# Kernel optimization log

Measured on AMD Instinct MI355X. Metric: run time of the kernel, lower is better.

Reference implementation:

```python
import jax, jax.numpy as jnp
import numpy as np

ALPHA = 0.9
BETA = 1.0  # theta=None, layer=None -> PyG GCN2Conv beta = 1.0
N_CONV = 2


def _gcn_norm(edge_index, edge_weight, num_nodes):
    # gcn_norm with add_self_loops=False: symmetric D^-1/2 A D^-1/2
    row, col = edge_index[0], edge_index[1]
    deg = jax.ops.segment_sum(edge_weight, col, num_segments=num_nodes)
    dinv = jnp.where(deg > 0, jax.lax.rsqrt(jnp.where(deg > 0, deg, 1.0)), 0.0)
    return dinv[row] * edge_weight * dinv[col]


def _gcn2_conv(h, x0, edge_index, norm_w, w1, num_nodes):
    row, col = edge_index[0], edge_index[1]
    msg = h[row] * norm_w[:, None]                     # gather + scale  [E, F]
    agg = jax.ops.segment_sum(msg, col, num_segments=num_nodes)  # scatter-add [N, F]
    out = (1.0 - ALPHA) * agg + ALPHA * x0             # initial residual
    return (1.0 - BETA) * out + BETA * (out @ w1)      # shared_weights=True path


def setup_inputs() -> dict:
    key = jax.random.key(0)
    ks = jax.random.split(key, 8)
    N, E, H, F = 100000, 1600000, 64, 64
    x = jax.random.normal(ks[0], (N, H), dtype=jnp.float32)
    edge_index = jax.random.randint(ks[1], (2, E), 0, N, dtype=jnp.int64)
    edge_weight = jax.random.uniform(ks[2], (E,), dtype=jnp.float32)
    edge_attr = jax.random.normal(ks[3], (E, 5), dtype=jnp.float32)
    lin0_w = jax.random.normal(ks[4], (F, H), dtype=jnp.float32) / np.sqrt(H)
    lin0_b = jnp.zeros((F,), dtype=jnp.float32)
    # per-conv GCN2Conv weight1 [n_conv, F, F]
    w1 = jax.random.normal(ks[5], (N_CONV, F, F), dtype=jnp.float32) / np.sqrt(F)
    return {"x": x, "edge_index": edge_index, "edge_weight": edge_weight,
            "edge_attr": edge_attr, "lin0_w": lin0_w, "lin0_b": lin0_b, "w1": w1}


def reference(x, edge_index, edge_weight, edge_attr, lin0_w, lin0_b, w1):
    del edge_attr  # unused by the module
    num_nodes = x.shape[0]
    h0 = jax.nn.relu(x @ lin0_w.T + lin0_b)
    norm_w = _gcn_norm(edge_index, edge_weight, num_nodes)
    out = h0
    for i in range(N_CONV):
        out = out + jax.nn.relu(_gcn2_conv(out, h0, edge_index, norm_w, w1[i], num_nodes))
    return out
```

## Files before the change

kernel.cpp:

```cpp
#include <hip/hip_runtime.h>
#include <hip/hip_fp16.h>

#define NN 100000
#define NE 1600000
#define H0_NB 1563
#define HBLK 256
#define EPB 6250
#define NBKT 196
#define CAP 9216

static __device__ __forceinline__ float bitsf(unsigned u) {
    union { unsigned u; float f; } t; t.u = u; return t.f;
}

static __device__ __forceinline__ unsigned short f2bf(float f) {
    union { float f; unsigned u; } t; t.f = f;
    unsigned r = t.u + 0x7fffu + ((t.u >> 16) & 1u);
    return (unsigned short)(r >> 16);
}

static __device__ __forceinline__ void ld_bf4(const unsigned short* p, float* f) {
    uint2 u = *reinterpret_cast<const uint2*>(p);
    f[0] = bitsf(u.x << 16);
    f[1] = bitsf(u.x & 0xffff0000u);
    f[2] = bitsf(u.y << 16);
    f[3] = bitsf(u.y & 0xffff0000u);
}

static __device__ __forceinline__ float ldf(const void* p, int i, int fb) {
    return fb ? bitsf(((unsigned)((const unsigned short*)p)[i]) << 16)
              : ((const float*)p)[i];
}

static __device__ __forceinline__ int ld_row(const int* ei, int e, int i64) {
    return i64 ? ei[2 * e] : ei[e];
}
static __device__ __forceinline__ int ld_col(const int* ei, int e, int i64) {
    return i64 ? ei[2 * NE + 2 * e] : ei[NE + e];
}

static __device__ __forceinline__ unsigned f16bits(float w) {
    __half h = __float2half_rn(w);
    union { __half h; unsigned short s; } t; t.h = h;
    return (unsigned)t.s;
}
static __device__ __forceinline__ float f16val(unsigned b) {
    union { __half h; unsigned short s; } t; t.s = (unsigned short)b;
    return __half2float(t.h);
}

__global__ void k_init(const unsigned short* __restrict__ xs, const int* __restrict__ ei,
                       int* __restrict__ flags, int* __restrict__ bktcnt) {
    __shared__ int s_bad[256], s_odd[256];
    int t = threadIdx.x;
    if (t < NBKT) bktcnt[t] = 0;
    int bad = 0;
    for (int i = 0; i < 16; i++) {
        unsigned short v = xs[t * 16 + i];
        if (((v >> 7) & 0xFF) >= 0xC0) bad++;
    }
    s_bad[t] = bad;
    s_odd[t] = (ei[2 * t + 1] != 0) ? 1 : 0;
    __syncthreads();
    if (t == 0) {
        int B = 0, O = 0;
        for (int i = 0; i < 256; i++) { B += s_bad[i]; O += s_odd[i]; }
        flags[0] = (B < 16) ? 1 : 0;
        flags[1] = (O == 0) ? 1 : 0;
    }
}

__global__ void k_scatterh0(const void* __restrict__ x, const void* __restrict__ w0,
                            const void* __restrict__ b0, unsigned short* __restrict__ h0b,
                            const int* __restrict__ ei, const void* __restrict__ ew,
                            int* __restrict__ bktcnt, unsigned* __restrict__ recs_cr,
                            unsigned short* __restrict__ recs_w,
                            const int* __restrict__ flags) {
    __shared__ float s_w[64 * 64];
    __shared__ float s_x[16 * 68];
    __shared__ unsigned s_cnt[NBKT];
    __shared__ unsigned s_cur[NBKT];
    int tid = threadIdx.x;
    int bb = blockIdx.x;

    if (bb < HBLK) {
        int i64 = flags[1], fb = flags[0];
        if (tid < NBKT) s_cnt[tid] = 0;
        __syncthreads();
        for (int i = tid; i < EPB; i += 256) {
            int c = ld_col(ei, bb * EPB + i, i64);
            atomicAdd(&s_cnt[c >> 9], 1u);
        }
        __syncthreads();
        if (tid < NBKT) {
            unsigned base = (unsigned)atomicAdd(&bktcnt[tid], (int)s_cnt[tid]);
            s_cur[tid] = (unsigned)tid * CAP + base;
        }
        __syncthreads();
        for (int i = tid; i < EPB; i += 256) {
            int e = bb * EPB + i;
            int c = ld_col(ei, e, i64);
            int r = ld_row(ei, e, i64);
            float w = ldf(ew, e, fb);
            unsigned pos = atomicAdd(&s_cur[c >> 9], 1u);
            if (pos < (unsigned)((c >> 9) + 1) * CAP) {
                recs_cr[pos] = ((unsigned)(c & 511) << 17) | (unsigned)r;
                recs_w[pos] = (unsigned short)f16bits(w);
            }
        }
        return;
    }

    int hb = bb - HBLK;
    int fb = flags[0];
    if (fb) {
        const unsigned short* wp = (const unsigned short*)w0;
#pragma unroll
        for (int i = 0; i < 16; i += 4) {
            int idx = tid * 16 + i;
            float wv[4]; ld_bf4(wp + idx, wv);
            int f = idx >> 6, k = idx & 63;
            s_w[(k + 0) * 64 + f] = wv[0];
            s_w[(k + 1) * 64 + f] = wv[1];
            s_w[(k + 2) * 64 + f] = wv[2];
            s_w[(k + 3) * 64 + f] = wv[3];
        }
    } else {
        const float* wp = (const float*)w0;
#pragma unroll
        for (int i = 0; i < 16; i += 4) {
            int idx = tid * 16 + i;
            float4 wv = *(const float4*)(wp + idx);
            int f = idx >> 6, k = idx & 63;
            s_w[(k + 0) * 64 + f] = wv.x;
            s_w[(k + 1) * 64 + f] = wv.y;
            s_w[(k + 2) * 64 + f] = wv.z;
            s_w[(k + 3) * 64 + f] = wv.w;
        }
    }

    int g = tid >> 4, q = tid & 15;
    float bias[4];
    if (fb) {
        ld_bf4((const unsigned short*)b0 + q * 4, bias);
    } else {
        float4 bv = *(const float4*)((const float*)b0 + q * 4);
        bias[0] = bv.x; bias[1] = bv.y; bias[2] = bv.z; bias[3] = bv.w;
    }

    for (int s = 0; s < 4; s++) {
        int n = hb * 64 + s * 16 + g;
        __syncthreads();
        if (n < NN) {
            float xv[4];
            if (fb) {
                ld_bf4((const unsigned short*)x + (size_t)n * 64 + q * 4, xv);
            } else {
                float4 t4 = *(const float4*)((const float*)x + (size_t)n * 64 + q * 4);
                xv[0] = t4.x; xv[1] = t4.y; xv[2] = t4.z; xv[3] = t4.w;
            }
            s_x[g * 68 + q * 4 + 0] = xv[0];
            s_x[g * 68 + q * 4 + 1] = xv[1];
            s_x[g * 68 + q * 4 + 2] = xv[2];
            s_x[g * 68 + q * 4 + 3] = xv[3];
        }
        __syncthreads();
        if (n >= NN) continue;

        float acc[4] = {0.f, 0.f, 0.f, 0.f};
#pragma unroll 8
        for (int k4 = 0; k4 < 64; k4 += 4) {
            float4 tq = *(const float4*)(&s_x[g * 68 + k4]);
            float4 w0v = *(const float4*)(&s_w[(k4 + 0) * 64 + q * 4]);
            float4 w1v = *(const float4*)(&s_w[(k4 + 1) * 64 + q * 4]);
            float4 w2v = *(const float4*)(&s_w[(k4 + 2) * 64 + q * 4]);
            float4 w3v = *(const float4*)(&s_w[(k4 + 3) * 64 + q * 4]);
            acc[0] += tq.x * w0v.x + tq.y * w1v.x + tq.z * w2v.x + tq.w * w3v.x;
            acc[1] += tq.x * w0v.y + tq.y * w1v.y + tq.z * w2v.y + tq.w * w3v.y;
            acc[2] += tq.x * w0v.z + tq.y * w1v.z + tq.z * w2v.z + tq.w * w3v.z;
            acc[3] += tq.x * w0v.w + tq.y * w1v.w + tq.z * w2v.w + tq.w * w3v.w;
        }
        ushort4 o;
        float v0 = acc[0] + bias[0]; o.x = f2bf(v0 > 0.f ? v0 : 0.f);
        float v1 = acc[1] + bias[1]; o.y = f2bf(v1 > 0.f ? v1 : 0.f);
        float v2 = acc[2] + bias[2]; o.z = f2bf(v2 > 0.f ? v2 : 0.f);
        float v3 = acc[3] + bias[3]; o.w = f2bf(v3 > 0.f ? v3 : 0.f);
        *(ushort4*)(h0b + (size_t)n * 64 + q * 4) = o;
    }
}

__global__ void __launch_bounds__(512)
k_bucket(const unsigned* __restrict__ recs_cr, const unsigned short* __restrict__ recs_w,
         const int* __restrict__ bktcnt,
         int* __restrict__ ptrg, float* __restrict__ dinvg, int* __restrict__ edgedata) {
    __shared__ unsigned s_srt[CAP];
    __shared__ unsigned s_c[512], s_s[512], s_cur[512];
    __shared__ int sb[NBKT + 1];
    int b = blockIdx.x, t = threadIdx.x;

    if (t < NBKT) {
        int v = bktcnt[t];
        sb[t] = (v > CAP) ? CAP : v;
    }
    __syncthreads();
    if (t == 0) {
        int run = 0;
        for (int i = 0; i < NBKT; i++) { int v = sb[i]; sb[i] = run; run += v; }
        sb[NBKT] = run;
    }
    __syncthreads();
    int jb = sb[b];
    int m = sb[b + 1] - jb;
    unsigned src = (unsigned)b * CAP;

    s_c[t] = 0;
    __syncthreads();
    for (int i = t; i < m; i += 512)
        atomicAdd(&s_c[recs_cr[src + i] >> 17], 1u);
    __syncthreads();
    s_s[t] = s_c[t];
    __syncthreads();
    for (int off = 1; off < 512; off <<= 1) {
        unsigned u = (t >= off) ? s_s[t - off] : 0u;
        __syncthreads();
        s_s[t] += u;
        __syncthreads();
    }
    unsigned exc = s_s[t] - s_c[t];
    s_cur[t] = exc;
    int c = (b << 9) + t;
    if (c < NN) ptrg[c] = jb + (int)exc;
    if (b == NBKT - 1 && t == 0) ptrg[NN] = sb[NBKT];
    __syncthreads();
    for (int i = t; i < m; i += 512) {
        unsigned cr = recs_cr[src + i];
        unsigned wv = (unsigned)recs_w[src + i] & 0x7fffu;
        unsigned pos = atomicAdd(&s_cur[cr >> 17], 1u);
        s_srt[pos] = ((cr & 0x1ffffu) << 15) | wv;
    }
    __syncthreads();
    if (c < NN) {
        float sum = 0.f;
        unsigned e1 = s_s[t];
        for (unsigned j = exc; j < e1; j++) sum += f16val(s_srt[j] & 0x7fffu);
        dinvg[c] = (sum > 0.f) ? rsqrtf(sum) : 0.f;
    }
    for (int i = t; i < m; i += 512) edgedata[jb + i] = (int)s_srt[i];
}

__global__ void k_conv(const int* __restrict__ ptrg, const float* __restrict__ dinvg,
                       const int* __restrict__ edgedata,
                       const unsigned short* __restrict__ cur_in,
                       const unsigned short* __restrict__ h0b,
                       const void* __restrict__ w1, void* __restrict__ cur_out,
                       int layer, const int* __restrict__ flags) {
    __shared__ float s_w[64 * 64];
    __shared__ float s_t[16 * 68];
    int fb = flags[0];
    int out_bf = fb ? 1 : (layer == 0);

    int tid = threadIdx.x;
    if (fb) {
        const unsigned short* wp = (const unsigned short*)w1 + layer * 4096;
        for (int i = 0; i < 16; i += 4) {
            int idx = tid * 16 + i;
            float wv[4]; ld_bf4(wp + idx, wv);
            s_w[idx] = wv[0]; s_w[idx + 1] = wv[1]; s_w[idx + 2] = wv[2]; s_w[idx + 3] = wv[3];
        }
    } else {
        const float* wp = (const float*)w1 + layer * 4096;
        for (int i = 0; i < 16; i += 4) {
            int idx = tid * 16 + i;
            float4 wv = *(const float4*)(wp + idx);
            s_w[idx] = wv.x; s_w[idx + 1] = wv.y; s_w[idx + 2] = wv.z; s_w[idx + 3] = wv.w;
        }
    }

    int g = tid >> 4, q = tid & 15;
    int lane = tid & 63;
    int gbase = lane & 48;
    int n = blockIdx.x * 16 + g;
    float acc[4] = {0.f, 0.f, 0.f, 0.f};
    if (n < NN) {
        int jb = ptrg[n], je = ptrg[n + 1];
        int deg = je - jb;
        float dn = dinvg[n];

        int nfull = deg & ~15;
        for (int j0 = jb; j0 < jb + nfull; j0 += 16) {
            int rec = __builtin_nontemporal_load(edgedata + j0 + q);
            int rq = ((unsigned)rec) >> 15;
            float wq = f16val((unsigned)rec & 0x7fffu) * dinvg[rq];
#pragma unroll
            for (int i = 0; i < 16; i++) {
                int r = __shfl(rq, gbase + i, 64);
                float w = __shfl(wq, gbase + i, 64);
                float hvv[4];
                ld_bf4(cur_in + (size_t)r * 64 + q * 4, hvv);
                acc[0] += hvv[0] * w; acc[1] += hvv[1] * w;
                acc[2] += hvv[2] * w; acc[3] += hvv[3] * w;
            }
        }
        int rem = deg - nfull;
        if (rem > 0) {
            int rq = 0; float wq = 0.f;
            if (q < rem) {
                int rec = __builtin_nontemporal_load(edgedata + jb + nfull + q);
                rq = ((unsigned)rec) >> 15;
                wq = f16val((unsigned)rec & 0x7fffu) * dinvg[rq];
            }
            for (int i = 0; i < rem; i++) {
                int r = __shfl(rq, gbase + i, 64);
                float w = __shfl(wq, gbase + i, 64);
                float hvv[4];
                ld_bf4(cur_in + (size_t)r * 64 + q * 4, hvv);
                acc[0] += hvv[0] * w; acc[1] += hvv[1] * w;
                acc[2] += hvv[2] * w; acc[3] += hvv[3] * w;
            }
        }
        float hv[4]; ld_bf4(h0b + (size_t)n * 64 + q * 4, hv);
#pragma unroll
        for (int j = 0; j < 4; j++)
            s_t[g * 68 + q * 4 + j] = 0.1f * (dn * acc[j]) + 0.9f * hv[j];
    }
    __syncthreads();
    if (n >= NN) return;

    float acc2[4] = {0.f, 0.f, 0.f, 0.f};
#pragma unroll 8
    for (int k = 0; k < 64; k++) {
        float tv = s_t[g * 68 + k];
        float4 wv = *(const float4*)(&s_w[k * 64 + q * 4]);
        acc2[0] += tv * wv.x; acc2[1] += tv * wv.y;
        acc2[2] += tv * wv.z; acc2[3] += tv * wv.w;
    }
    float c[4];
    ld_bf4(cur_in + (size_t)n * 64 + q * 4, c);
#pragma unroll
    for (int j = 0; j < 4; j++) c[j] += (acc2[j] > 0.f) ? acc2[j] : 0.f;
    if (out_bf) {
        ushort4 o;
        o.x = f2bf(c[0]); o.y = f2bf(c[1]); o.z = f2bf(c[2]); o.w = f2bf(c[3]);
        unsigned short* op = (unsigned short*)cur_out + (size_t)n * 64 + q * 4;
        if (layer == 1) {
            union { ushort4 s; unsigned long long u; } ou; ou.s = o;
            __builtin_nontemporal_store(ou.u, (unsigned long long*)op);
        } else {
            *(ushort4*)op = o;
        }
    } else {
        float4 o; o.x = c[0]; o.y = c[1]; o.z = c[2]; o.w = c[3];
        *(float4*)((float*)cur_out + (size_t)n * 64 + q * 4) = o;
    }
}

extern "C" void kernel_launch(void* const* d_in, const int* in_sizes, int n_in,
                              void* d_out, int out_size, void* d_ws, size_t ws_size,
                              hipStream_t stream) {
    (void)in_sizes; (void)n_in; (void)out_size; (void)ws_size;

    const void* x  = d_in[0];
    const int*  ei = (const int*)d_in[1];
    const void* ew = d_in[2];
    const void* w0 = d_in[4];
    const void* b0 = d_in[5];
    const void* w1 = d_in[6];

    char* wsb = (char*)d_ws;
    int*      flags    = (int*)wsb;
    int*      bktcnt   = (int*)(wsb + 256);
    int*      ptrg     = (int*)(wsb + 1280);
    float*    dinvg    = (float*)(wsb + 1280 + 400016);
    int*      edgedata = (int*)(wsb + 1280 + 400016 + 400000);
    unsigned short* h0b  = (unsigned short*)((char*)edgedata + 6400000);
    unsigned short* curB = h0b + (size_t)NN * 64;
    unsigned*       recs_cr = (unsigned*)curB;
    unsigned short* recs_w  = (unsigned short*)((char*)curB + 7225344);

    k_init<<<1, 256, 0, stream>>>((const unsigned short*)x, ei, flags, bktcnt);
    k_scatterh0<<<HBLK + H0_NB, 256, 0, stream>>>(x, w0, b0, h0b, ei, ew,
                                                  bktcnt, recs_cr, recs_w, flags);
    k_bucket<<<NBKT, 512, 0, stream>>>(recs_cr, recs_w, bktcnt, ptrg, dinvg, edgedata);

    int grid = (NN + 15) / 16;
    k_conv<<<grid, 256, 0, stream>>>(ptrg, dinvg, edgedata, h0b, h0b, w1, curB, 0, flags);
    k_conv<<<grid, 256, 0, stream>>>(ptrg, dinvg, edgedata, curB, h0b, w1, d_out, 1, flags);
}
```

Before: 317.1 us.

## Gather neighbor features from FP8 e4m3 copies and store dinv as fp16

Each node's feature row is also written as a packed FP8 e4m3 copy (h0 and layer-0 output). The conv kernels gather neighbor rows from this 64-byte copy instead of the 128-byte bf16 row, roughly halving the random-gather traffic. The degree-normalization array is also shrunk to fp16. This costs extra software encode/decode ALU work and a much coarser precision for messages, which may push the result beyond tolerance. Negative values from layer 0 outputs are not handled by the encoder, which assumes non-negative inputs.

```diff
diff --git a/kernel.cpp b/kernel.cpp
--- a/kernel.cpp
+++ b/kernel.cpp
@@ -12,6 +12,9 @@
 static __device__ __forceinline__ float bitsf(unsigned u) {
     union { unsigned u; float f; } t; t.u = u; return t.f;
 }
+static __device__ __forceinline__ unsigned fbits(float f) {
+    union { float f; unsigned u; } t; t.f = f; return t.u;
+}
 
 static __device__ __forceinline__ unsigned short f2bf(float f) {
     union { float f; unsigned u; } t; t.f = f;
@@ -47,6 +50,29 @@
 static __device__ __forceinline__ float f16val(unsigned b) {
     union { __half h; unsigned short s; } t; t.s = (unsigned short)b;
     return __half2float(t.h);
+}
+
+static __device__ __forceinline__ unsigned f2e4m3(float v) {
+    if (v >= 432.f) return 0x7Eu;
+    unsigned u = fbits(v);
+    int e = (int)(u >> 23) - 127;
+    if (e >= -6) {
+        unsigned keep = (u >> 20) & 7u;
+        unsigned rest = u & 0xfffffu;
+        unsigned rnd  = (rest > 0x80000u) || (rest == 0x80000u && (keep & 1u));
+        return (((unsigned)(e + 7) << 3) | keep) + rnd;
+    }
+    float s = v * 512.f;
+    unsigned M = (unsigned)s;
+    float fr = s - (float)M;
+    M += (fr > 0.5f) || (fr == 0.5f && (M & 1u));
+    return M;
+}
+static __device__ __forceinline__ float e4m3f(unsigned c) {
+    unsigned E = c >> 3, M = c & 7u;
+    float norm = bitsf(((E + 120u) << 23) | (M << 20));
+    float sub  = (float)M * 0.001953125f;
+    return E ? norm : sub;
 }
 
 __global__ void k_init(const unsigned short* __restrict__ xs, const int* __restrict__ ei,
@@ -72,6 +98,7 @@
 
 __global__ void k_scatterh0(const void* __restrict__ x, const void* __restrict__ w0,
                             const void* __restrict__ b0, unsigned short* __restrict__ h0b,
+                            unsigned* __restrict__ h0f8,
                             const int* __restrict__ ei, const void* __restrict__ ew,
                             int* __restrict__ bktcnt, unsigned* __restrict__ recs_cr,
                             unsigned short* __restrict__ recs_w,
@@ -180,19 +207,23 @@
             acc[2] += tq.x * w0v.z + tq.y * w1v.z + tq.z * w2v.z + tq.w * w3v.z;
             acc[3] += tq.x * w0v.w + tq.y * w1v.w + tq.z * w2v.w + tq.w * w3v.w;
         }
+        float r0 = acc[0] + bias[0]; r0 = (r0 > 0.f) ? r0 : 0.f;
+        float r1 = acc[1] + bias[1]; r1 = (r1 > 0.f) ? r1 : 0.f;
+        float r2 = acc[2] + bias[2]; r2 = (r2 > 0.f) ? r2 : 0.f;
+        float r3 = acc[3] + bias[3]; r3 = (r3 > 0.f) ? r3 : 0.f;
         ushort4 o;
-        float v0 = acc[0] + bias[0]; o.x = f2bf(v0 > 0.f ? v0 : 0.f);
-        float v1 = acc[1] + bias[1]; o.y = f2bf(v1 > 0.f ? v1 : 0.f);
-        float v2 = acc[2] + bias[2]; o.z = f2bf(v2 > 0.f ? v2 : 0.f);
-        float v3 = acc[3] + bias[3]; o.w = f2bf(v3 > 0.f ? v3 : 0.f);
+        o.x = f2bf(r0); o.y = f2bf(r1); o.z = f2bf(r2); o.w = f2bf(r3);
         *(ushort4*)(h0b + (size_t)n * 64 + q * 4) = o;
+        h0f8[(size_t)n * 16 + q] = f2e4m3(r0) | (f2e4m3(r1) << 8)
+                                 | (f2e4m3(r2) << 16) | (f2e4m3(r3) << 24);
     }
 }
 
 __global__ void __launch_bounds__(512)
 k_bucket(const unsigned* __restrict__ recs_cr, const unsigned short* __restrict__ recs_w,
          const int* __restrict__ bktcnt,
-         int* __restrict__ ptrg, float* __restrict__ dinvg, int* __restrict__ edgedata) {
+         int* __restrict__ ptrg, unsigned short* __restrict__ dinv16,
+         int* __restrict__ edgedata) {
     __shared__ unsigned s_srt[CAP];
     __shared__ unsigned s_c[512], s_s[512], s_cur[512];
     __shared__ int sb[NBKT + 1];
@@ -243,16 +274,19 @@
         float sum = 0.f;
         unsigned e1 = s_s[t];
         for (unsigned j = exc; j < e1; j++) sum += f16val(s_srt[j] & 0x7fffu);
-        dinvg[c] = (sum > 0.f) ? rsqrtf(sum) : 0.f;
+        float dr = (sum > 0.f) ? rsqrtf(sum) : 0.f;
+        dinv16[c] = (unsigned short)f16bits(dr);
     }
     for (int i = t; i < m; i += 512) edgedata[jb + i] = (int)s_srt[i];
 }
 
-__global__ void k_conv(const int* __restrict__ ptrg, const float* __restrict__ dinvg,
+__global__ void k_conv(const int* __restrict__ ptrg, const unsigned short* __restrict__ dinv16,
                        const int* __restrict__ edgedata,
                        const unsigned short* __restrict__ cur_in,
+                       const unsigned* __restrict__ gf8,
                        const unsigned short* __restrict__ h0b,
                        const void* __restrict__ w1, void* __restrict__ cur_out,
+                       unsigned* __restrict__ outf8,
                        int layer, const int* __restrict__ flags) {
     __shared__ float s_w[64 * 64];
     __shared__ float s_t[16 * 68];
@@ -284,21 +318,22 @@
     if (n < NN) {
         int jb = ptrg[n], je = ptrg[n + 1];
         int deg = je - jb;
-        float dn = dinvg[n];
+        float dn = f16val(dinv16[n]);
 
         int nfull = deg & ~15;
         for (int j0 = jb; j0 < jb + nfull; j0 += 16) {
             int rec = __builtin_nontemporal_load(edgedata + j0 + q);
             int rq = ((unsigned)rec) >> 15;
-            float wq = f16val((unsigned)rec & 0x7fffu) * dinvg[rq];
+            float wq = f16val((unsigned)rec & 0x7fffu) * f16val(dinv16[rq]);
 #pragma unroll
             for (int i = 0; i < 16; i++) {
                 int r = __shfl(rq, gbase + i, 64);
                 float w = __shfl(wq, gbase + i, 64);
-                float hvv[4];
-                ld_bf4(cur_in + (size_t)r * 64 + q * 4, hvv);
-                acc[0] += hvv[0] * w; acc[1] += hvv[1] * w;
-                acc[2] += hvv[2] * w; acc[3] += hvv[3] * w;
+                unsigned pv = gf8[(size_t)r * 16 + q];
+                acc[0] += e4m3f(pv & 0xffu) * w;
+                acc[1] += e4m3f((pv >> 8) & 0xffu) * w;
+                acc[2] += e4m3f((pv >> 16) & 0xffu) * w;
+                acc[3] += e4m3f(pv >> 24) * w;
             }
         }
         int rem = deg - nfull;
@@ -307,15 +342,16 @@
             if (q < rem) {
                 int rec = __builtin_nontemporal_load(edgedata + jb + nfull + q);
                 rq = ((unsigned)rec) >> 15;
-                wq = f16val((unsigned)rec & 0x7fffu) * dinvg[rq];
+                wq = f16val((unsigned)rec & 0x7fffu) * f16val(dinv16[rq]);
             }
             for (int i = 0; i < rem; i++) {
                 int r = __shfl(rq, gbase + i, 64);
                 float w = __shfl(wq, gbase + i, 64);
-                float hvv[4];
-                ld_bf4(cur_in + (size_t)r * 64 + q * 4, hvv);
-                acc[0] += hvv[0] * w; acc[1] += hvv[1] * w;
-                acc[2] += hvv[2] * w; acc[3] += hvv[3] * w;
+                unsigned pv = gf8[(size_t)r * 16 + q];
+                acc[0] += e4m3f(pv & 0xffu) * w;
+                acc[1] += e4m3f((pv >> 8) & 0xffu) * w;
+                acc[2] += e4m3f((pv >> 16) & 0xffu) * w;
+                acc[3] += e4m3f(pv >> 24) * w;
             }
         }
         float hv[4]; ld_bf4(h0b + (size_t)n * 64 + q * 4, hv);
@@ -338,6 +374,9 @@
     ld_bf4(cur_in + (size_t)n * 64 + q * 4, c);
 #pragma unroll
     for (int j = 0; j < 4; j++) c[j] += (acc2[j] > 0.f) ? acc2[j] : 0.f;
+    if (outf8)
+        outf8[(size_t)n * 16 + q] = f2e4m3(c[0]) | (f2e4m3(c[1]) << 8)
+                                  | (f2e4m3(c[2]) << 16) | (f2e4m3(c[3]) << 24);
     if (out_bf) {
         ushort4 o;
         o.x = f2bf(c[0]); o.y = f2bf(c[1]); o.z = f2bf(c[2]); o.w = f2bf(c[3]);
@@ -367,22 +406,26 @@
     const void* w1 = d_in[6];
 
     char* wsb = (char*)d_ws;
-    int*      flags    = (int*)wsb;
-    int*      bktcnt   = (int*)(wsb + 256);
-    int*      ptrg     = (int*)(wsb + 1280);
-    float*    dinvg    = (float*)(wsb + 1280 + 400016);
-    int*      edgedata = (int*)(wsb + 1280 + 400016 + 400000);
-    unsigned short* h0b  = (unsigned short*)((char*)edgedata + 6400000);
-    unsigned short* curB = h0b + (size_t)NN * 64;
-    unsigned*       recs_cr = (unsigned*)curB;
-    unsigned short* recs_w  = (unsigned short*)((char*)curB + 7225344);
+    int*            flags    = (int*)wsb;
+    int*            bktcnt   = (int*)(wsb + 64);
+    int*            ptrg     = (int*)(wsb + 848);
+    unsigned short* dinv16   = (unsigned short*)(wsb + 400852);
+    int*            edgedata = (int*)(wsb + 600852);
+    unsigned*       h0f8     = (unsigned*)(wsb + 7000852);
+    unsigned short* h0b      = (unsigned short*)(wsb + 13400856);
+    unsigned short* curB     = (unsigned short*)(wsb + 26200856);
+    unsigned*       curf8    = (unsigned*)(wsb + 39000856);
+    unsigned*       recs_cr  = (unsigned*)(wsb + 26200856);
+    unsigned short* recs_w   = (unsigned short*)(wsb + 33426200);
 
     k_init<<<1, 256, 0, stream>>>((const unsigned short*)x, ei, flags, bktcnt);
-    k_scatterh0<<<HBLK + H0_NB, 256, 0, stream>>>(x, w0, b0, h0b, ei, ew,
+    k_scatterh0<<<HBLK + H0_NB, 256, 0, stream>>>(x, w0, b0, h0b, h0f8, ei, ew,
                                                   bktcnt, recs_cr, recs_w, flags);
-    k_bucket<<<NBKT, 512, 0, stream>>>(recs_cr, recs_w, bktcnt, ptrg, dinvg, edgedata);
+    k_bucket<<<NBKT, 512, 0, stream>>>(recs_cr, recs_w, bktcnt, ptrg, dinv16, edgedata);
 
     int grid = (NN + 15) / 16;
-    k_conv<<<grid, 256, 0, stream>>>(ptrg, dinvg, edgedata, h0b, h0b, w1, curB, 0, flags);
-    k_conv<<<grid, 256, 0, stream>>>(ptrg, dinvg, edgedata, curB, h0b, w1, d_out, 1, flags);
-}
+    k_conv<<<grid, 256, 0, stream>>>(ptrg, dinv16, edgedata, h0b, h0f8, h0b,
+                                     w1, curB, curf8, 0, flags);
+    k_conv<<<grid, 256, 0, stream>>>(ptrg, dinv16, edgedata, curB, curf8, h0b,
+                                     w1, d_out, nullptr, 1, flags);
+}
```

Measured after the change: 370.9 us. 17.0% more time.
